# Kernel optimization log

Hardware: AMD Instinct MI355X
Metric: run time of the kernel (lower is better)

## Reference

```python
import jax, jax.numpy as jnp
import numpy as np

B, V, DEMB, H, LAT, L = 16384, 64, 128, 512, 128, 2
PAD, BOS, EOS = 0, 1, 2


def setup_inputs() -> dict:
    key = jax.random.key(0)
    ks = jax.random.split(key, 12)
    s = 0.05  # small init so softmax logits stay well-scaled
    z = jax.random.normal(ks[0], (B, LAT), jnp.float32)
    E = jax.random.normal(ks[1], (V, DEMB), jnp.float32) * s
    E = E.at[PAD].set(0.0)  # padding_idx row is zero
    W_l2h = jax.random.normal(ks[2], (H, LAT), jnp.float32) * s
    b_l2h = jnp.zeros((H,), jnp.float32)
    W_ih0 = jax.random.normal(ks[3], (4 * H, DEMB), jnp.float32) * s
    W_hh0 = jax.random.normal(ks[4], (4 * H, H), jnp.float32) * s
    b_ih0 = jnp.zeros((4 * H,), jnp.float32)
    b_hh0 = jnp.zeros((4 * H,), jnp.float32)
    W_ih1 = jax.random.normal(ks[5], (4 * H, H), jnp.float32) * s
    W_hh1 = jax.random.normal(ks[6], (4 * H, H), jnp.float32) * s
    b_ih1 = jnp.zeros((4 * H,), jnp.float32)
    b_hh1 = jnp.zeros((4 * H,), jnp.float32)
    W_out = jax.random.normal(ks[7], (V, H), jnp.float32) * s
    b_out = jnp.zeros((V,), jnp.float32)
    return {"z": z, "E": E, "W_l2h": W_l2h, "b_l2h": b_l2h,
            "W_ih0": W_ih0, "W_hh0": W_hh0, "b_ih0": b_ih0, "b_hh0": b_hh0,
            "W_ih1": W_ih1, "W_hh1": W_hh1, "b_ih1": b_ih1, "b_hh1": b_hh1,
            "W_out": W_out, "b_out": b_out, "max_len": 100}


def _lstm_cell(x, h, c, Wih, Whh, bih, bhh):
    # torch LSTM gate order: i, f, g, o
    g = x @ Wih.T + bih + h @ Whh.T + bhh  # [B, 4H]
    i, f, gg, o = jnp.split(g, 4, axis=-1)
    c_new = jax.nn.sigmoid(f) * c + jax.nn.sigmoid(i) * jnp.tanh(gg)
    h_new = jax.nn.sigmoid(o) * jnp.tanh(c_new)
    return h_new, c_new


def reference(z, E, W_l2h, b_l2h, W_ih0, W_hh0, b_ih0, b_hh0,
              W_ih1, W_hh1, b_ih1, b_hh1, W_out, b_out, max_len):
    # initial states: c0 = latent2hidden(z) repeated over layers, h0 = 0
    c0 = z @ W_l2h.T + b_l2h                      # [B, H]
    c = jnp.stack([c0, c0])                       # [L, B, H]
    h = jnp.zeros_like(c)
    prev = jnp.full((B,), BOS, jnp.int32)
    is_end = jnp.zeros((B,), bool)
    keys = jax.random.split(jax.random.key(42), max_len)

    def step(carry, k):
        h, c, prev, is_end = carry
        x = E[prev]                               # [B, DEMB]
        h0, c0_ = _lstm_cell(x, h[0], c[0], W_ih0, W_hh0, b_ih0, b_hh0)
        h1, c1_ = _lstm_cell(h0, h[1], c[1], W_ih1, W_hh1, b_ih1, b_hh1)
        logits = h1 @ W_out.T + b_out             # [B, V]
        cur = jax.random.categorical(k, logits)   # same dist as Categorical(softmax(logits))
        is_end = is_end | (cur == EOS)            # mark eos; eos itself becomes pad
        cur = jnp.where(is_end, PAD, cur).astype(jnp.int32)
        return (jnp.stack([h0, h1]), jnp.stack([c0_, c1_]), cur, is_end), cur

    _, samples = jax.lax.scan(step, (h, c, prev, is_end), keys)  # [T, B]
    return samples.T                              # [B, T]
```

## Files before the change

### kernel.cpp

```cpp
#include <hip/hip_runtime.h>
#include <stdint.h>

#define B_    16384
#define V_    64
#define DEMB_ 128
#define H_    512
#define PAD_  0
#define BOS_  1
#define EOS_  2

__device__ __forceinline__ uint32_t rotl32(uint32_t v, int n) {
    return (v << n) | (v >> (32 - n));
}

__device__ __forceinline__ void tf2x32(uint32_t k0, uint32_t k1,
                                       uint32_t x0, uint32_t x1,
                                       uint32_t& o0, uint32_t& o1)
{
    const uint32_t k2 = k0 ^ k1 ^ 0x1BD11BDAu;
    x0 += k0; x1 += k1;
#define TFR(r) { x0 += x1; x1 = rotl32(x1, (r)); x1 ^= x0; }
    TFR(13) TFR(15) TFR(26) TFR(6)
    x0 += k1; x1 += k2 + 1u;
    TFR(17) TFR(29) TFR(16) TFR(24)
    x0 += k2; x1 += k0 + 2u;
    TFR(13) TFR(15) TFR(26) TFR(6)
    x0 += k0; x1 += k1 + 3u;
    TFR(17) TFR(29) TFR(16) TFR(24)
    x0 += k1; x1 += k2 + 4u;
    TFR(13) TFR(15) TFR(26) TFR(6)
    x0 += k2; x1 += k0 + 5u;
#undef TFR
    o0 = x0; o1 = x1;
}

__device__ __forceinline__ float sigm(float x) {
    return 1.0f / (1.0f + expf(-x));
}

__global__ __launch_bounds__(256)
void init_state(const float* __restrict__ z, const float* __restrict__ Wl,
                const float* __restrict__ bl,
                float* __restrict__ C0, float* __restrict__ C1,
                float* __restrict__ H0, float* __restrict__ H1)
{
    __shared__ __align__(16) float As[16][68];
    __shared__ __align__(16) float Bs[16][68];
    const int tid  = threadIdx.x;
    const int b0   = blockIdx.x * 64;
    const int j0   = blockIdx.y * 64;
    const int tx   = tid & 15, ty = tid >> 4;
    const int lrow = tid >> 2, lkq = tid & 3;

    float acc[4][4] = {};

    for (int kt = 0; kt < DEMB_ / 16; ++kt) {
        const int k0 = kt * 16;
        float4 av = *reinterpret_cast<const float4*>(z  + (size_t)(b0 + lrow) * DEMB_ + k0 + lkq * 4);
        float4 bv = *reinterpret_cast<const float4*>(Wl + (size_t)(j0 + lrow) * DEMB_ + k0 + lkq * 4);
        __syncthreads();
        As[lkq*4+0][lrow] = av.x; As[lkq*4+1][lrow] = av.y; As[lkq*4+2][lrow] = av.z; As[lkq*4+3][lrow] = av.w;
        Bs[lkq*4+0][lrow] = bv.x; Bs[lkq*4+1][lrow] = bv.y; Bs[lkq*4+2][lrow] = bv.z; Bs[lkq*4+3][lrow] = bv.w;
        __syncthreads();
#pragma unroll
        for (int kk = 0; kk < 16; ++kk) {
            float4 a4 = *reinterpret_cast<const float4*>(&As[kk][ty*4]);
            float4 b4 = *reinterpret_cast<const float4*>(&Bs[kk][tx*4]);
            float ar[4] = {a4.x, a4.y, a4.z, a4.w};
            float br[4] = {b4.x, b4.y, b4.z, b4.w};
#pragma unroll
            for (int r = 0; r < 4; ++r)
#pragma unroll
                for (int c = 0; c < 4; ++c)
                    acc[r][c] = fmaf(ar[r], br[c], acc[r][c]);
        }
    }

#pragma unroll
    for (int r = 0; r < 4; ++r) {
        const int b = b0 + ty * 4 + r;
        const int j = j0 + tx * 4;
        float v0 = acc[r][0] + bl[j+0];
        float v1 = acc[r][1] + bl[j+1];
        float v2 = acc[r][2] + bl[j+2];
        float v3 = acc[r][3] + bl[j+3];
        float4 cv = {v0, v1, v2, v3};
        float4 zz = {0.f, 0.f, 0.f, 0.f};
        *reinterpret_cast<float4*>(C0 + (size_t)b * H_ + j) = cv;
        *reinterpret_cast<float4*>(C1 + (size_t)b * H_ + j) = cv;
        *reinterpret_cast<float4*>(H0 + (size_t)b * H_ + j) = zz;
        *reinterpret_cast<float4*>(H1 + (size_t)b * H_ + j) = zz;
    }
}

__global__ __launch_bounds__(256)
void init_tokens(int* __restrict__ prevtok, int* __restrict__ isend)
{
    int i = blockIdx.x * 256 + threadIdx.x;
    if (i < B_) { prevtok[i] = BOS_; isend[i] = 0; }
}

template<int KX, bool GATHER>
__global__ __launch_bounds__(256)
void lstm_layer(const float* __restrict__ Asrc,
                const int*   __restrict__ prevtok,
                const float* __restrict__ Hrec,
                const float* __restrict__ Wih,
                const float* __restrict__ Whh,
                const float* __restrict__ bih,
                const float* __restrict__ bhh,
                float* __restrict__ Cst,
                float* __restrict__ Hout)
{
    __shared__ __align__(16) float As[16][68];
    __shared__ __align__(16) float Bs[4][16][68];
    __shared__ int rowtok[64];

    const int tid  = threadIdx.x;
    const int b0   = blockIdx.x * 64;
    const int j0   = blockIdx.y * 64;
    const int tx   = tid & 15, ty = tid >> 4;
    const int lrow = tid >> 2, lkq = tid & 3;

    if (GATHER) {
        if (tid < 64) rowtok[tid] = prevtok[b0 + tid];
    }
    __syncthreads();

    float acc[4][4][4] = {};

    const int NT = (KX + H_) / 16;
    for (int kt = 0; kt < NT; ++kt) {
        const int k0 = kt * 16;
        float4 av;
        float4 bv[4];
        if (k0 < KX) {
            const float* arow = GATHER ? (Asrc + (size_t)rowtok[lrow] * DEMB_)
                                       : (Asrc + (size_t)(b0 + lrow) * KX);
            av = *reinterpret_cast<const float4*>(arow + k0 + lkq * 4);
#pragma unroll
            for (int g = 0; g < 4; ++g)
                bv[g] = *reinterpret_cast<const float4*>(
                    Wih + (size_t)(g * H_ + j0 + lrow) * KX + k0 + lkq * 4);
        } else {
            const int kh = k0 - KX;
            av = *reinterpret_cast<const float4*>(Hrec + (size_t)(b0 + lrow) * H_ + kh + lkq * 4);
#pragma unroll
            for (int g = 0; g < 4; ++g)
                bv[g] = *reinterpret_cast<const float4*>(
                    Whh + (size_t)(g * H_ + j0 + lrow) * H_ + kh + lkq * 4);
        }
        __syncthreads();
        As[lkq*4+0][lrow] = av.x; As[lkq*4+1][lrow] = av.y; As[lkq*4+2][lrow] = av.z; As[lkq*4+3][lrow] = av.w;
#pragma unroll
        for (int g = 0; g < 4; ++g) {
            Bs[g][lkq*4+0][lrow] = bv[g].x; Bs[g][lkq*4+1][lrow] = bv[g].y;
            Bs[g][lkq*4+2][lrow] = bv[g].z; Bs[g][lkq*4+3][lrow] = bv[g].w;
        }
        __syncthreads();
#pragma unroll
        for (int kk = 0; kk < 16; ++kk) {
            float4 a4 = *reinterpret_cast<const float4*>(&As[kk][ty*4]);
            float ar[4] = {a4.x, a4.y, a4.z, a4.w};
#pragma unroll
            for (int g = 0; g < 4; ++g) {
                float4 b4 = *reinterpret_cast<const float4*>(&Bs[g][kk][tx*4]);
                float br[4] = {b4.x, b4.y, b4.z, b4.w};
#pragma unroll
                for (int r = 0; r < 4; ++r)
#pragma unroll
                    for (int c = 0; c < 4; ++c)
                        acc[g][r][c] = fmaf(ar[r], br[c], acc[g][r][c]);
            }
        }
    }

    const int j = j0 + tx * 4;
#pragma unroll
    for (int r = 0; r < 4; ++r) {
        const int b = b0 + ty * 4 + r;
        float4 c4 = *reinterpret_cast<const float4*>(Cst + (size_t)b * H_ + j);
        float cold[4] = {c4.x, c4.y, c4.z, c4.w};
        float cn[4], hn[4];
#pragma unroll
        for (int c = 0; c < 4; ++c) {
            const int n = j + c;
            float gi = acc[0][r][c] + bih[n]          + bhh[n];
            float gf = acc[1][r][c] + bih[H_ + n]     + bhh[H_ + n];
            float gg = acc[2][r][c] + bih[2*H_ + n]   + bhh[2*H_ + n];
            float go = acc[3][r][c] + bih[3*H_ + n]   + bhh[3*H_ + n];
            float si = sigm(gi), sf = sigm(gf), so = sigm(go);
            float tg = tanhf(gg);
            float cc = __fadd_rn(__fmul_rn(sf, cold[c]), __fmul_rn(si, tg));
            cn[c] = cc;
            hn[c] = __fmul_rn(so, tanhf(cc));
        }
        float4 co = {cn[0], cn[1], cn[2], cn[3]};
        float4 ho = {hn[0], hn[1], hn[2], hn[3]};
        *reinterpret_cast<float4*>(Cst  + (size_t)b * H_ + j) = co;
        *reinterpret_cast<float4*>(Hout + (size_t)b * H_ + j) = ho;
    }
}

__global__ __launch_bounds__(256)
void sample_step(const float* __restrict__ H1src, const float* __restrict__ Wout,
                 const float* __restrict__ bout,
                 int* __restrict__ prevtok, int* __restrict__ isend,
                 int* __restrict__ out, int t, int T)
{
    __shared__ __align__(16) float As[16][68];
    __shared__ __align__(16) float Bs[16][68];
    __shared__ float LG[64][65];

    const int tid  = threadIdx.x;
    const int b0   = blockIdx.x * 64;
    const int tx   = tid & 15, ty = tid >> 4;
    const int lrow = tid >> 2, lkq = tid & 3;

    float acc[4][4] = {};

    for (int kt = 0; kt < H_ / 16; ++kt) {
        const int k0 = kt * 16;
        float4 av = *reinterpret_cast<const float4*>(H1src + (size_t)(b0 + lrow) * H_ + k0 + lkq * 4);
        float4 bv = *reinterpret_cast<const float4*>(Wout  + (size_t)lrow * H_ + k0 + lkq * 4);
        __syncthreads();
        As[lkq*4+0][lrow] = av.x; As[lkq*4+1][lrow] = av.y; As[lkq*4+2][lrow] = av.z; As[lkq*4+3][lrow] = av.w;
        Bs[lkq*4+0][lrow] = bv.x; Bs[lkq*4+1][lrow] = bv.y; Bs[lkq*4+2][lrow] = bv.z; Bs[lkq*4+3][lrow] = bv.w;
        __syncthreads();
#pragma unroll
        for (int kk = 0; kk < 16; ++kk) {
            float4 a4 = *reinterpret_cast<const float4*>(&As[kk][ty*4]);
            float4 b4 = *reinterpret_cast<const float4*>(&Bs[kk][tx*4]);
            float ar[4] = {a4.x, a4.y, a4.z, a4.w};
            float br[4] = {b4.x, b4.y, b4.z, b4.w};
#pragma unroll
            for (int r = 0; r < 4; ++r)
#pragma unroll
                for (int c = 0; c < 4; ++c)
                    acc[r][c] = fmaf(ar[r], br[c], acc[r][c]);
        }
    }

#pragma unroll
    for (int r = 0; r < 4; ++r)
#pragma unroll
        for (int c = 0; c < 4; ++c)
            LG[ty*4 + r][tx*4 + c] = acc[r][c] + bout[tx*4 + c];
    __syncthreads();

    const int wv = tid >> 6, lane = tid & 63;
    uint32_t kt0, kt1;
    tf2x32(0u, 42u, 0u, (uint32_t)t, kt0, kt1);

    const float TINY = 1.1754943508222875e-38f;
    for (int rr = 0; rr < 16; ++rr) {
        const int r = wv * 16 + rr;
        const int b = b0 + r;
        float lg = LG[r][lane];
        uint32_t r0, r1;
        tf2x32(kt0, kt1, 0u, (uint32_t)(b * V_ + lane), r0, r1);
        uint32_t bits = r0 ^ r1;
        float f = __uint_as_float((bits >> 9) | 0x3f800000u) - 1.0f;
        float u = fmaxf(TINY, __fadd_rn(f, TINY));
        float g = -logf(-logf(u));
        float val = __fadd_rn(g, lg);
        int idx = lane;
#pragma unroll
        for (int off = 32; off > 0; off >>= 1) {
            float ov = __shfl_xor(val, off, 64);
            int   oi = __shfl_xor(idx, off, 64);
            if (ov > val || (ov == val && oi < idx)) { val = ov; idx = oi; }
        }
        if (lane == 0) {
            int cur = idx;
            int e   = isend[b];
            int en  = e | (cur == EOS_);
            int tok = en ? PAD_ : cur;
            isend[b]   = en;
            prevtok[b] = tok;
            out[(size_t)b * T + t] = tok;
        }
    }
}

extern "C" void kernel_launch(void* const* d_in, const int* in_sizes, int n_in,
                              void* d_out, int out_size, void* d_ws, size_t ws_size,
                              hipStream_t stream)
{
    (void)in_sizes; (void)n_in; (void)ws_size;
    const float* z    = (const float*)d_in[0];
    const float* E    = (const float*)d_in[1];
    const float* Wl2h = (const float*)d_in[2];
    const float* bl2h = (const float*)d_in[3];
    const float* Wih0 = (const float*)d_in[4];
    const float* Whh0 = (const float*)d_in[5];
    const float* bih0 = (const float*)d_in[6];
    const float* bhh0 = (const float*)d_in[7];
    const float* Wih1 = (const float*)d_in[8];
    const float* Whh1 = (const float*)d_in[9];
    const float* bih1 = (const float*)d_in[10];
    const float* bhh1 = (const float*)d_in[11];
    const float* Wout = (const float*)d_in[12];
    const float* bout = (const float*)d_in[13];
    int* out = (int*)d_out;
    const int T = out_size / B_;

    char* w = (char*)d_ws;
    const size_t S = (size_t)B_ * H_ * sizeof(float);
    float* C0  = (float*)(w + 0 * S);
    float* C1  = (float*)(w + 1 * S);
    float* H0A = (float*)(w + 2 * S);
    float* H0B = (float*)(w + 3 * S);
    float* H1A = (float*)(w + 4 * S);
    float* H1B = (float*)(w + 5 * S);
    int* prevtok = (int*)(w + 6 * S);
    int* isend   = (int*)(w + 6 * S + (size_t)B_ * sizeof(int));

    dim3 blk(256);
    init_state<<<dim3(B_/64, H_/64), blk, 0, stream>>>(z, Wl2h, bl2h, C0, C1, H0A, H1A);
    init_tokens<<<dim3(B_/256), blk, 0, stream>>>(prevtok, isend);

    float *h0c = H0A, *h0n = H0B, *h1c = H1A, *h1n = H1B;
    for (int t = 0; t < T; ++t) {
        lstm_layer<DEMB_, true><<<dim3(B_/64, H_/64), blk, 0, stream>>>(
            E, prevtok, h0c, Wih0, Whh0, bih0, bhh0, C0, h0n);
        lstm_layer<H_, false><<<dim3(B_/64, H_/64), blk, 0, stream>>>(
            h0n, nullptr, h1c, Wih1, Whh1, bih1, bhh1, C1, h1n);
        sample_step<<<dim3(B_/64), blk, 0, stream>>>(
            h1n, Wout, bout, prevtok, isend, out, t, T);
        float* tmp;
        tmp = h0c; h0c = h0n; h0n = tmp;
        tmp = h1c; h1c = h1n; h1n = tmp;
    }
}
```

Baseline: 137.7 ms.

## Enlarge LSTM GEMM tile to 128 rows with register-prefetched global loads

The fused LSTM gate kernel now computes a 128x64 (x4 gates) output tile per block, with each thread holding 8x4x4 accumulators, which doubles reuse of each weight tile loaded into shared memory. The next k-slice is loaded from global memory into registers while the current slice is being multiplied, and the bias vectors are loaded once as float4 before the epilogue. Register pressure roughly doubles, and launch bounds request two blocks per CU, which may force spills or reduce occupancy.

Measured after the change: 134.1 ms. -2.7%, faster.

```diff
diff --git a/kernel.cpp b/kernel.cpp
--- a/kernel.cpp
+++ b/kernel.cpp
@@ -101,7 +101,7 @@
 }
 
 template<int KX, bool GATHER>
-__global__ __launch_bounds__(256)
+__global__ __launch_bounds__(256, 2)
 void lstm_layer(const float* __restrict__ Asrc,
                 const int*   __restrict__ prevtok,
                 const float* __restrict__ Hrec,
@@ -112,62 +112,110 @@
                 float* __restrict__ Cst,
                 float* __restrict__ Hout)
 {
-    __shared__ __align__(16) float As[16][68];
+    __shared__ __align__(16) float As[16][132];
     __shared__ __align__(16) float Bs[4][16][68];
-    __shared__ int rowtok[64];
+    __shared__ int rowtok[128];
 
     const int tid  = threadIdx.x;
-    const int b0   = blockIdx.x * 64;
+    const int b0   = blockIdx.x * 128;
     const int j0   = blockIdx.y * 64;
-    const int tx   = tid & 15, ty = tid >> 4;
-    const int lrow = tid >> 2, lkq = tid & 3;
+    const int tx   = tid & 15;
+    const int ty   = tid >> 4;
+    const int srow = tid >> 1;
+    const int sk   = (tid & 1) * 8;
 
     if (GATHER) {
-        if (tid < 64) rowtok[tid] = prevtok[b0 + tid];
-    }
-    __syncthreads();
-
-    float acc[4][4][4] = {};
+        if (tid < 128) rowtok[tid] = prevtok[b0 + tid];
+        __syncthreads();
+    }
 
     const int NT = (KX + H_) / 16;
+
+    float4 av[2], bv[4];
+    {
+        const int k0 = 0;
+        const float* arow = GATHER ? (Asrc + (size_t)rowtok[srow] * DEMB_)
+                                   : (Asrc + (size_t)(b0 + srow) * KX);
+        av[0] = *reinterpret_cast<const float4*>(arow + k0 + sk);
+        av[1] = *reinterpret_cast<const float4*>(arow + k0 + sk + 4);
+#pragma unroll
+        for (int h = 0; h < 2; ++h) {
+            const int grow = srow + h * 128;
+            const int g = grow >> 6, u = grow & 63;
+            const float* brow = Wih + (size_t)(g * H_ + j0 + u) * KX + k0 + sk;
+            bv[h*2+0] = *reinterpret_cast<const float4*>(brow);
+            bv[h*2+1] = *reinterpret_cast<const float4*>(brow + 4);
+        }
+    }
+
+    float acc[4][8][4] = {};
+
     for (int kt = 0; kt < NT; ++kt) {
-        const int k0 = kt * 16;
-        float4 av;
-        float4 bv[4];
-        if (k0 < KX) {
-            const float* arow = GATHER ? (Asrc + (size_t)rowtok[lrow] * DEMB_)
-                                       : (Asrc + (size_t)(b0 + lrow) * KX);
-            av = *reinterpret_cast<const float4*>(arow + k0 + lkq * 4);
-#pragma unroll
-            for (int g = 0; g < 4; ++g)
-                bv[g] = *reinterpret_cast<const float4*>(
-                    Wih + (size_t)(g * H_ + j0 + lrow) * KX + k0 + lkq * 4);
-        } else {
-            const int kh = k0 - KX;
-            av = *reinterpret_cast<const float4*>(Hrec + (size_t)(b0 + lrow) * H_ + kh + lkq * 4);
-#pragma unroll
-            for (int g = 0; g < 4; ++g)
-                bv[g] = *reinterpret_cast<const float4*>(
-                    Whh + (size_t)(g * H_ + j0 + lrow) * H_ + kh + lkq * 4);
-        }
-        __syncthreads();
-        As[lkq*4+0][lrow] = av.x; As[lkq*4+1][lrow] = av.y; As[lkq*4+2][lrow] = av.z; As[lkq*4+3][lrow] = av.w;
-#pragma unroll
-        for (int g = 0; g < 4; ++g) {
-            Bs[g][lkq*4+0][lrow] = bv[g].x; Bs[g][lkq*4+1][lrow] = bv[g].y;
-            Bs[g][lkq*4+2][lrow] = bv[g].z; Bs[g][lkq*4+3][lrow] = bv[g].w;
-        }
-        __syncthreads();
-#pragma unroll
+        __syncthreads();
+        {
+            float a0[4] = {av[0].x, av[0].y, av[0].z, av[0].w};
+            float a1[4] = {av[1].x, av[1].y, av[1].z, av[1].w};
+#pragma unroll
+            for (int i = 0; i < 4; ++i) {
+                As[sk + i][srow]     = a0[i];
+                As[sk + 4 + i][srow] = a1[i];
+            }
+#pragma unroll
+            for (int h = 0; h < 2; ++h) {
+                const int grow = srow + h * 128;
+                const int g = grow >> 6, u = grow & 63;
+                float b0r[4] = {bv[h*2+0].x, bv[h*2+0].y, bv[h*2+0].z, bv[h*2+0].w};
+                float b1r[4] = {bv[h*2+1].x, bv[h*2+1].y, bv[h*2+1].z, bv[h*2+1].w};
+#pragma unroll
+                for (int i = 0; i < 4; ++i) {
+                    Bs[g][sk + i][u]     = b0r[i];
+                    Bs[g][sk + 4 + i][u] = b1r[i];
+                }
+            }
+        }
+        __syncthreads();
+
+        if (kt + 1 < NT) {
+            const int k0n = (kt + 1) * 16;
+            if (k0n < KX) {
+                const float* arow = GATHER ? (Asrc + (size_t)rowtok[srow] * DEMB_)
+                                           : (Asrc + (size_t)(b0 + srow) * KX);
+                av[0] = *reinterpret_cast<const float4*>(arow + k0n + sk);
+                av[1] = *reinterpret_cast<const float4*>(arow + k0n + sk + 4);
+#pragma unroll
+                for (int h = 0; h < 2; ++h) {
+                    const int grow = srow + h * 128;
+                    const int g = grow >> 6, u = grow & 63;
+                    const float* brow = Wih + (size_t)(g * H_ + j0 + u) * KX + k0n + sk;
+                    bv[h*2+0] = *reinterpret_cast<const float4*>(brow);
+                    bv[h*2+1] = *reinterpret_cast<const float4*>(brow + 4);
+                }
+            } else {
+                const int kh = k0n - KX;
+                av[0] = *reinterpret_cast<const float4*>(Hrec + (size_t)(b0 + srow) * H_ + kh + sk);
+                av[1] = *reinterpret_cast<const float4*>(Hrec + (size_t)(b0 + srow) * H_ + kh + sk + 4);
+#pragma unroll
+                for (int h = 0; h < 2; ++h) {
+                    const int grow = srow + h * 128;
+                    const int g = grow >> 6, u = grow & 63;
+                    const float* brow = Whh + (size_t)(g * H_ + j0 + u) * H_ + kh + sk;
+                    bv[h*2+0] = *reinterpret_cast<const float4*>(brow);
+                    bv[h*2+1] = *reinterpret_cast<const float4*>(brow + 4);
+                }
+            }
+        }
+
+#pragma unroll 4
         for (int kk = 0; kk < 16; ++kk) {
-            float4 a4 = *reinterpret_cast<const float4*>(&As[kk][ty*4]);
-            float ar[4] = {a4.x, a4.y, a4.z, a4.w};
+            float4 a40 = *reinterpret_cast<const float4*>(&As[kk][ty*8]);
+            float4 a41 = *reinterpret_cast<const float4*>(&As[kk][ty*8+4]);
+            float ar[8] = {a40.x, a40.y, a40.z, a40.w, a41.x, a41.y, a41.z, a41.w};
 #pragma unroll
             for (int g = 0; g < 4; ++g) {
                 float4 b4 = *reinterpret_cast<const float4*>(&Bs[g][kk][tx*4]);
                 float br[4] = {b4.x, b4.y, b4.z, b4.w};
 #pragma unroll
-                for (int r = 0; r < 4; ++r)
+                for (int r = 0; r < 8; ++r)
 #pragma unroll
                     for (int c = 0; c < 4; ++c)
                         acc[g][r][c] = fmaf(ar[r], br[c], acc[g][r][c]);
@@ -176,19 +224,31 @@
     }
 
     const int j = j0 + tx * 4;
-#pragma unroll
-    for (int r = 0; r < 4; ++r) {
-        const int b = b0 + ty * 4 + r;
+    float4 bi0 = *reinterpret_cast<const float4*>(bih + 0*H_ + j);
+    float4 bi1 = *reinterpret_cast<const float4*>(bih + 1*H_ + j);
+    float4 bi2 = *reinterpret_cast<const float4*>(bih + 2*H_ + j);
+    float4 bi3 = *reinterpret_cast<const float4*>(bih + 3*H_ + j);
+    float4 bh0 = *reinterpret_cast<const float4*>(bhh + 0*H_ + j);
+    float4 bh1 = *reinterpret_cast<const float4*>(bhh + 1*H_ + j);
+    float4 bh2 = *reinterpret_cast<const float4*>(bhh + 2*H_ + j);
+    float4 bh3 = *reinterpret_cast<const float4*>(bhh + 3*H_ + j);
+    float bi[4][4] = {{bi0.x,bi0.y,bi0.z,bi0.w},{bi1.x,bi1.y,bi1.z,bi1.w},
+                      {bi2.x,bi2.y,bi2.z,bi2.w},{bi3.x,bi3.y,bi3.z,bi3.w}};
+    float bh[4][4] = {{bh0.x,bh0.y,bh0.z,bh0.w},{bh1.x,bh1.y,bh1.z,bh1.w},
+                      {bh2.x,bh2.y,bh2.z,bh2.w},{bh3.x,bh3.y,bh3.z,bh3.w}};
+
+#pragma unroll
+    for (int r = 0; r < 8; ++r) {
+        const int b = b0 + ty * 8 + r;
         float4 c4 = *reinterpret_cast<const float4*>(Cst + (size_t)b * H_ + j);
         float cold[4] = {c4.x, c4.y, c4.z, c4.w};
         float cn[4], hn[4];
 #pragma unroll
         for (int c = 0; c < 4; ++c) {
-            const int n = j + c;
-            float gi = acc[0][r][c] + bih[n]          + bhh[n];
-            float gf = acc[1][r][c] + bih[H_ + n]     + bhh[H_ + n];
-            float gg = acc[2][r][c] + bih[2*H_ + n]   + bhh[2*H_ + n];
-            float go = acc[3][r][c] + bih[3*H_ + n]   + bhh[3*H_ + n];
+            float gi = acc[0][r][c] + bi[0][c] + bh[0][c];
+            float gf = acc[1][r][c] + bi[1][c] + bh[1][c];
+            float gg = acc[2][r][c] + bi[2][c] + bh[2][c];
+            float go = acc[3][r][c] + bi[3][c] + bh[3][c];
             float si = sigm(gi), sf = sigm(gf), so = sigm(go);
             float tg = tanhf(gg);
             float cc = __fadd_rn(__fmul_rn(sf, cold[c]), __fmul_rn(si, tg));
@@ -322,9 +382,9 @@
 
     float *h0c = H0A, *h0n = H0B, *h1c = H1A, *h1n = H1B;
     for (int t = 0; t < T; ++t) {
-        lstm_layer<DEMB_, true><<<dim3(B_/64, H_/64), blk, 0, stream>>>(
+        lstm_layer<DEMB_, true><<<dim3(B_/128, H_/64), blk, 0, stream>>>(
             E, prevtok, h0c, Wih0, Whh0, bih0, bhh0, C0, h0n);
-        lstm_layer<H_, false><<<dim3(B_/64, H_/64), blk, 0, stream>>>(
+        lstm_layer<H_, false><<<dim3(B_/128, H_/64), blk, 0, stream>>>(
             h0n, nullptr, h1c, Wih1, Whh1, bih1, bhh1, C1, h1n);
         sample_step<<<dim3(B_/64), blk, 0, stream>>>(
             h1n, Wout, bout, prevtok, isend, out, t, T);
```
